# Kernel tuning notes

Measured on AMD Instinct MI355X. Metric: run time of the kernel, lower is better.

## Reference

```python
import jax, jax.numpy as jnp
import numpy as np

INV_DELTA = 15.0  # init kwarg inv_delta
EPS = 1e-12       # torch F.normalize eps


def setup_inputs() -> dict:
    key = jax.random.key(0)
    k1, k2 = jax.random.split(key)
    features = jax.random.normal(k1, (32, 256, 30, 30), dtype=jnp.float32)
    # _embedding buffer: randn clamped to >= 0
    embedding = jnp.maximum(jax.random.normal(k2, (2048, 256), dtype=jnp.float32), 0.0)
    # _min_distance_mean buffer, initialized to 0.5
    min_distance_mean = jnp.ones((1,), dtype=jnp.float32) * 0.5
    return {"features": features, "embedding": embedding,
            "min_distance_mean": min_distance_mean}


def reference(features, embedding, min_distance_mean):
    # crop 1-pixel border: [B,C,H,W] -> [B,C,H-2,W-2]
    f = features[:, :, 1:-1, 1:-1]
    # squared euclidean distance to each codeword via GEMM trick:
    # dist[b,k,h,w] = ||f[b,:,h,w]||^2 + ||e[k]||^2 - 2 <f, e[k]>
    f2 = jnp.sum(f * f, axis=1, keepdims=True)                 # [B,1,H',W']
    e2 = jnp.sum(embedding * embedding, axis=1)                # [K]
    xe = jnp.einsum('bchw,kc->bkhw', f, embedding)             # 1x1-conv GEMM
    dist = f2 + e2[None, :, None, None] - 2.0 * xe             # [B,K,H',W']
    # adaptive temperature softmax over codewords
    inv_delta_adaptive = INV_DELTA / min_distance_mean[0]
    codes = jax.nn.softmax(-inv_delta_adaptive * dist, axis=1)  # [B,K,H',W']
    # global average pool + L1 normalize
    bow = jnp.mean(codes, axis=(2, 3))                          # [B,K]
    bow = bow / jnp.maximum(jnp.sum(jnp.abs(bow), axis=1, keepdims=True), EPS)
    return (bow, codes)
```

## Files before the change

kernel.cpp:

```cpp
#include <hip/hip_runtime.h>
#include <hip/hip_bf16.h>
#include <math.h>

typedef __attribute__((ext_vector_type(8))) short bf16x8;
typedef __attribute__((ext_vector_type(16))) float f32x16;

#define B_ 32
#define C_ 256
#define K_ 2048
#define HW_ 784
#define NPIX 25088
#define FEAT_BSTRIDE 230400
#define FEAT_CSTRIDE 900
#define INV_DELTA 15.0f
#define LOG2E 1.4426950408889634f
#define QSCALE 409.6f
#define QDEC (LOG2E / QSCALE)

#define BM 128
#define BN 128
#define LSTR 40
#define NSLAB 16

__device__ __forceinline__ ushort f2bf(float x) {
    __hip_bfloat16 h = __float2bfloat16(x);
    return *reinterpret_cast<ushort*>(&h);
}
__device__ __forceinline__ float bf2f(ushort u) {
    __hip_bfloat16 h;
    *reinterpret_cast<ushort*>(&h) = u;
    return __bfloat162float(h);
}

__global__ void e2_kernel(const float* __restrict__ emb, float* __restrict__ e2) {
    int t = threadIdx.x;
    int wid = t >> 6, lane = t & 63;
    int k = blockIdx.x * 4 + wid;
    const float* er = emb + (size_t)k * C_;
    float v0 = er[lane], v1 = er[lane + 64], v2 = er[lane + 128], v3 = er[lane + 192];
    float s = v0 * v0 + v1 * v1 + v2 * v2 + v3 * v3;
#pragma unroll
    for (int off = 32; off > 0; off >>= 1) s += __shfl_xor(s, off);
    if (lane == 0) e2[k] = s;
}

__global__ void prep_e_kernel(const float* __restrict__ emb,
                              ushort* __restrict__ ehi, ushort* __restrict__ elo) {
    int i = blockIdx.x * 256 + threadIdx.x;
    float v = emb[i];
    ushort h = f2bf(v);
    float r = v - bf2f(h);
    ehi[i] = h;
    elo[i] = f2bf(r);
}

__global__ __launch_bounds__(256, 2) void gemm_kernel(
    const float* __restrict__ feat, const ushort* __restrict__ ehi,
    const ushort* __restrict__ elo, const float* __restrict__ mdm,
    const float* __restrict__ e2g, ushort* __restrict__ zq,
    float* __restrict__ m_part, float* __restrict__ l_part)
{
    __shared__ ushort Ah[BM * LSTR], Al[BM * LSTR], Bh[BN * LSTR], Bl[BN * LSTR];
    __shared__ float redA[2][132];
    __shared__ float redM[132];

    int t = threadIdx.x;
    int lane = t & 63, wid = t >> 6;
    int wrow = wid >> 1, wcol = wid & 1;
    int g = lane >> 5, ci = lane & 31;

    int px0 = blockIdx.x * BM;
    int k0  = blockIdx.y * BN;

    int apx = t & 127;
    int ahalf = t >> 7;
    int pxs = px0 + apx;
    int bs = pxs / HW_, hws = pxs % HW_;
    int hs = hws / 28, wsx = hws % 28;
    const float* fbase = feat + (size_t)bs * FEAT_BSTRIDE + (size_t)(hs + 1) * 30 + (wsx + 1);

    f32x16 acc[2][2];
#pragma unroll
    for (int mi = 0; mi < 2; ++mi)
#pragma unroll
        for (int ni = 0; ni < 2; ++ni)
            acc[mi][ni] = (f32x16)(0.0f);

    for (int kc = 0; kc < 8; ++kc) {
        int c0 = kc * 32;
        __syncthreads();
        {
            float v[16];
#pragma unroll
            for (int p = 0; p < 16; ++p)
                v[p] = fbase[(size_t)(c0 + ahalf * 16 + p) * FEAT_CSTRIDE];
#pragma unroll
            for (int o = 0; o < 2; ++o) {
                uint4 uh, ul;
                uint* uhp = reinterpret_cast<uint*>(&uh);
                uint* ulp = reinterpret_cast<uint*>(&ul);
#pragma unroll
                for (int q = 0; q < 4; ++q) {
                    float f0 = v[o * 8 + 2 * q], f1 = v[o * 8 + 2 * q + 1];
                    ushort h0 = f2bf(f0), h1 = f2bf(f1);
                    float r0 = f0 - bf2f(h0), r1 = f1 - bf2f(h1);
                    uhp[q] = (uint)h0 | ((uint)h1 << 16);
                    ulp[q] = (uint)f2bf(r0) | ((uint)f2bf(r1) << 16);
                }
                int oct = ahalf * 2 + o;
                *reinterpret_cast<uint4*>(&Ah[apx * LSTR + oct * 8]) = uh;
                *reinterpret_cast<uint4*>(&Al[apx * LSTR + oct * 8]) = ul;
            }
        }
        {
#pragma unroll
            for (int i = 0; i < 2; ++i) {
                int idx = t + i * 256;
                int kl = idx >> 2, oct = idx & 3;
                uint4 vh = *reinterpret_cast<const uint4*>(&ehi[(size_t)(k0 + kl) * C_ + c0 + oct * 8]);
                uint4 vl = *reinterpret_cast<const uint4*>(&elo[(size_t)(k0 + kl) * C_ + c0 + oct * 8]);
                *reinterpret_cast<uint4*>(&Bh[kl * LSTR + oct * 8]) = vh;
                *reinterpret_cast<uint4*>(&Bl[kl * LSTR + oct * 8]) = vl;
            }
        }
        __syncthreads();
#pragma unroll
        for (int s = 0; s < 2; ++s) {
            bf16x8 ah[2], av[2], bh[2], bv[2];
#pragma unroll
            for (int mi = 0; mi < 2; ++mi) {
                int off = (wrow * 64 + mi * 32 + ci) * LSTR + s * 16 + g * 8;
                ah[mi] = *reinterpret_cast<const bf16x8*>(&Ah[off]);
                av[mi] = *reinterpret_cast<const bf16x8*>(&Al[off]);
            }
#pragma unroll
            for (int ni = 0; ni < 2; ++ni) {
                int off = (wcol * 64 + ni * 32 + ci) * LSTR + s * 16 + g * 8;
                bh[ni] = *reinterpret_cast<const bf16x8*>(&Bh[off]);
                bv[ni] = *reinterpret_cast<const bf16x8*>(&Bl[off]);
            }
#pragma unroll
            for (int mi = 0; mi < 2; ++mi)
#pragma unroll
                for (int ni = 0; ni < 2; ++ni) {
                    acc[mi][ni] = __builtin_amdgcn_mfma_f32_32x32x16_bf16(ah[mi], bh[ni], acc[mi][ni], 0, 0, 0);
                    acc[mi][ni] = __builtin_amdgcn_mfma_f32_32x32x16_bf16(ah[mi], bv[ni], acc[mi][ni], 0, 0, 0);
                    acc[mi][ni] = __builtin_amdgcn_mfma_f32_32x32x16_bf16(av[mi], bh[ni], acc[mi][ni], 0, 0, 0);
                }
        }
    }

    const float alpha = INV_DELTA / mdm[0];
    float e2v[2];
#pragma unroll
    for (int ni = 0; ni < 2; ++ni) e2v[ni] = e2g[k0 + wcol * 64 + ni * 32 + ci];
#pragma unroll
    for (int mi = 0; mi < 2; ++mi)
#pragma unroll
        for (int ni = 0; ni < 2; ++ni)
            acc[mi][ni] = alpha * (2.0f * acc[mi][ni] - e2v[ni]);

    float ms[2][16];
    {
        float mt[2][16];
#pragma unroll
        for (int mi = 0; mi < 2; ++mi)
#pragma unroll
            for (int r = 0; r < 16; ++r)
                mt[mi][r] = fmaxf(acc[mi][0][r], acc[mi][1][r]);
#pragma unroll
        for (int off = 1; off < 32; off <<= 1)
#pragma unroll
            for (int mi = 0; mi < 2; ++mi)
#pragma unroll
                for (int r = 0; r < 16; ++r)
                    mt[mi][r] = fmaxf(mt[mi][r], __shfl_xor(mt[mi][r], off));
        if (ci == 0) {
#pragma unroll
            for (int mi = 0; mi < 2; ++mi)
#pragma unroll
                for (int r = 0; r < 16; ++r)
                    redA[wcol][wrow * 64 + mi * 32 + (r & 3) + 8 * (r >> 2) + 4 * g] = mt[mi][r];
        }
    }
    __syncthreads();
    if (t < 128) redM[t] = fmaxf(redA[0][t], redA[1][t]);
    __syncthreads();
#pragma unroll
    for (int mi = 0; mi < 2; ++mi)
#pragma unroll
        for (int r = 0; r < 16; ++r)
            ms[mi][r] = redM[wrow * 64 + mi * 32 + (r & 3) + 8 * (r >> 2) + 4 * g];

    {
        float lt[2][16];
#pragma unroll
        for (int mi = 0; mi < 2; ++mi)
#pragma unroll
            for (int r = 0; r < 16; ++r)
                lt[mi][r] = exp2f((acc[mi][0][r] - ms[mi][r]) * LOG2E) +
                            exp2f((acc[mi][1][r] - ms[mi][r]) * LOG2E);
#pragma unroll
        for (int off = 1; off < 32; off <<= 1)
#pragma unroll
            for (int mi = 0; mi < 2; ++mi)
#pragma unroll
                for (int r = 0; r < 16; ++r)
                    lt[mi][r] += __shfl_xor(lt[mi][r], off);
        if (ci == 0) {
#pragma unroll
            for (int mi = 0; mi < 2; ++mi)
#pragma unroll
                for (int r = 0; r < 16; ++r)
                    redA[wcol][wrow * 64 + mi * 32 + (r & 3) + 8 * (r >> 2) + 4 * g] = lt[mi][r];
        }
    }
    __syncthreads();
    if (t < 128) {
        int slab = blockIdx.y;
        m_part[(size_t)slab * NPIX + px0 + t] = redM[t];
        l_part[(size_t)slab * NPIX + px0 + t] = redA[0][t] + redA[1][t];
    }

#pragma unroll
    for (int mi = 0; mi < 2; ++mi)
#pragma unroll
        for (int ni = 0; ni < 2; ++ni) {
            int k = k0 + wcol * 64 + ni * 32 + ci;
#pragma unroll
            for (int r = 0; r < 16; r += 2) {
                int row = wrow * 64 + mi * 32 + (r & 3) + 8 * (r >> 2) + 4 * g;
                int pxx = px0 + row;
                int bb = pxx / HW_, hh = pxx - bb * HW_;
                float s0 = fmaxf((acc[mi][ni][r]     - ms[mi][r])     * QSCALE, -32760.f);
                float s1 = fmaxf((acc[mi][ni][r + 1] - ms[mi][r + 1]) * QSCALE, -32760.f);
                int q0 = (int)s0, q1 = (int)s1;
                uint u = ((uint)(ushort)(short)q0) | (((uint)(ushort)(short)q1) << 16);
                *reinterpret_cast<uint*>(&zq[(size_t)(bb * K_ + k) * HW_ + hh]) = u;
            }
        }
}

__global__ void combine_kernel(const float* __restrict__ m_part, const float* __restrict__ l_part,
                               float* __restrict__ m_fin, float* __restrict__ rl_g) {
    int p = blockIdx.x * 256 + threadIdx.x;
    float m = -3.4e38f;
#pragma unroll
    for (int s = 0; s < NSLAB; ++s) m = fmaxf(m, m_part[(size_t)s * NPIX + p]);
    float l = 0.f;
#pragma unroll
    for (int s = 0; s < NSLAB; ++s)
        l += l_part[(size_t)s * NPIX + p] * exp2f((m_part[(size_t)s * NPIX + p] - m) * LOG2E);
    m_fin[p] = m;
    rl_g[p] = 1.0f / l;
}

__global__ __launch_bounds__(256) void finish_kernel(
    const ushort* __restrict__ zq, const float* __restrict__ m_part,
    const float* __restrict__ m_fin, const float* __restrict__ rl_g,
    float* __restrict__ codes, float* __restrict__ bow)
{
    __shared__ float corr[HW_], rls[HW_];
    __shared__ float bsum[64][4];
    int t = threadIdx.x;
    int kc = blockIdx.x, b = blockIdx.y;
    int slab = kc >> 1;
    for (int i = t; i < HW_; i += 256) {
        int p = b * HW_ + i;
        corr[i] = (m_part[(size_t)slab * NPIX + p] - m_fin[p]) * LOG2E;
        rls[i] = rl_g[p];
    }
    __syncthreads();
    int wid = t >> 6, lane = t & 63;
    for (int kl = 0; kl < 64; ++kl) {
        int k = kc * 64 + kl;
        size_t base = ((size_t)b * K_ + k) * HW_;
        float ssum = 0.f;
        if (t < 196) {
            uint2 raw = *reinterpret_cast<const uint2*>(&zq[base + t * 4]);
            int q0 = (int)(short)(raw.x & 0xffffu), q1 = (int)(short)(raw.x >> 16);
            int q2 = (int)(short)(raw.y & 0xffffu), q3 = (int)(short)(raw.y >> 16);
            float4 out;
            out.x = exp2f(fmaf((float)q0, QDEC, corr[t * 4 + 0])) * rls[t * 4 + 0];
            out.y = exp2f(fmaf((float)q1, QDEC, corr[t * 4 + 1])) * rls[t * 4 + 1];
            out.z = exp2f(fmaf((float)q2, QDEC, corr[t * 4 + 2])) * rls[t * 4 + 2];
            out.w = exp2f(fmaf((float)q3, QDEC, corr[t * 4 + 3])) * rls[t * 4 + 3];
            *reinterpret_cast<float4*>(&codes[base + t * 4]) = out;
            ssum = out.x + out.y + out.z + out.w;
        }
#pragma unroll
        for (int off = 32; off > 0; off >>= 1) ssum += __shfl_xor(ssum, off);
        if (lane == 0) bsum[kl][wid] = ssum;
    }
    __syncthreads();
    if (t < 64) {
        float s = bsum[t][0] + bsum[t][1] + bsum[t][2] + bsum[t][3];
        bow[(size_t)b * K_ + kc * 64 + t] = s * (1.0f / 784.0f);
    }
}

__global__ void bownorm_kernel(float* __restrict__ bow) {
    __shared__ float wred[4];
    __shared__ float denom_s;
    int b = blockIdx.x, t = threadIdx.x;
    float* row = bow + (size_t)b * K_;
    float v[8];
    float s = 0.f;
#pragma unroll
    for (int i = 0; i < 8; ++i) {
        v[i] = row[t + i * 256];
        s += fabsf(v[i]);
    }
#pragma unroll
    for (int off = 32; off > 0; off >>= 1) s += __shfl_xor(s, off);
    int wid = t >> 6, lane = t & 63;
    if (lane == 0) wred[wid] = s;
    __syncthreads();
    if (t == 0) denom_s = fmaxf(wred[0] + wred[1] + wred[2] + wred[3], 1e-12f);
    __syncthreads();
    float denom = denom_s;
#pragma unroll
    for (int i = 0; i < 8; ++i) row[t + i * 256] = v[i] / denom;
}

extern "C" void kernel_launch(void* const* d_in, const int* in_sizes, int n_in,
                              void* d_out, int out_size, void* d_ws, size_t ws_size,
                              hipStream_t stream) {
    const float* feat = (const float*)d_in[0];
    const float* emb  = (const float*)d_in[1];
    const float* mdm  = (const float*)d_in[2];
    float* bow   = (float*)d_out;
    float* codes = bow + (size_t)B_ * K_;

    char* ws = (char*)d_ws;
    size_t off = 0;
    auto alloc = [&](size_t bytes) { char* p = ws + off; off = (off + bytes + 255) & ~(size_t)255; return p; };
    ushort* ehi   = (ushort*)alloc((size_t)K_ * C_ * 2);
    ushort* elo   = (ushort*)alloc((size_t)K_ * C_ * 2);
    float*  e2    = (float*)alloc(K_ * 4);
    float*  m_part = (float*)alloc((size_t)NSLAB * NPIX * 4);
    float*  l_part = (float*)alloc((size_t)NSLAB * NPIX * 4);
    float*  m_fin = (float*)alloc((size_t)NPIX * 4);
    float*  rl_g  = (float*)alloc((size_t)NPIX * 4);
    ushort* zq    = (ushort*)alloc((size_t)NPIX * K_ * 2);

    e2_kernel<<<512, 256, 0, stream>>>(emb, e2);
    prep_e_kernel<<<2048, 256, 0, stream>>>(emb, ehi, elo);
    gemm_kernel<<<dim3(196, 16), 256, 0, stream>>>(feat, ehi, elo, mdm, e2, zq, m_part, l_part);
    combine_kernel<<<98, 256, 0, stream>>>(m_part, l_part, m_fin, rl_g);
    finish_kernel<<<dim3(32, 32), 256, 0, stream>>>(zq, m_part, m_fin, rl_g, codes, bow);
    bownorm_kernel<<<32, 256, 0, stream>>>(bow);
}
```

Measured before the change: 259.5 us.

## Pre-split features to bf16 hi/lo and stream GEMM tiles via direct global-to-LDS loads

Adds a prep kernel that transposes the cropped features into pixel-major bf16 hi/lo arrays, stored temporarily in the codes output buffer. The GEMM then loads all A and B tiles with global_load_lds into XOR-swizzled LDS rows of 64 elements, using a K-step of 64 channels. This replaces the strided fp32 gathers and the split conversion that were repeated in each of the 16 k-slab blocks. The block index is also remapped so that slabs sharing a pixel tile are scheduled together for L2 reuse. The cost is an extra kernel pass and larger LDS tiles, which may lower occupancy.

```diff
diff --git a/kernel.cpp b/kernel.cpp
--- a/kernel.cpp
+++ b/kernel.cpp
@@ -19,8 +19,11 @@
 
 #define BM 128
 #define BN 128
-#define LSTR 40
+#define LSTR 64
 #define NSLAB 16
+
+#define AS1 __attribute__((address_space(1)))
+#define AS3 __attribute__((address_space(3)))
 
 __device__ __forceinline__ ushort f2bf(float x) {
     __hip_bfloat16 h = __float2bfloat16(x);
@@ -30,6 +33,9 @@
     __hip_bfloat16 h;
     *reinterpret_cast<ushort*>(&h) = u;
     return __bfloat162float(h);
+}
+__device__ __forceinline__ void gl_lds16(const ushort* g, ushort* l) {
+    __builtin_amdgcn_global_load_lds((AS1 const uint*)g, (AS3 uint*)l, 16, 0, 0);
 }
 
 __global__ void e2_kernel(const float* __restrict__ emb, float* __restrict__ e2) {
@@ -54,13 +60,53 @@
     elo[i] = f2bf(r);
 }
 
+__global__ __launch_bounds__(256) void prep_f_kernel(const float* __restrict__ feat,
+                                                     ushort* __restrict__ fhi,
+                                                     ushort* __restrict__ flo) {
+    __shared__ float F[256 * 65];
+    int t = threadIdx.x;
+    int px0 = blockIdx.x * 64;
+    {
+        int lane = t & 63, cq = t >> 6;
+        int px = px0 + lane;
+        int b = px / HW_, hw = px % HW_;
+        int h = hw / 28, w = hw % 28;
+        const float* base = feat + (size_t)b * FEAT_BSTRIDE + (size_t)(h + 1) * 30 + (w + 1);
+#pragma unroll
+        for (int cc = 0; cc < 64; ++cc) {
+            int c = cq * 64 + cc;
+            F[c * 65 + lane] = base[(size_t)c * FEAT_CSTRIDE];
+        }
+    }
+    __syncthreads();
+    {
+        int px_l = t >> 2, cseg = t & 3;
+        size_t ob = (size_t)(px0 + px_l) * C_ + cseg * 64;
+        uint uh[32], ul[32];
+#pragma unroll
+        for (int j = 0; j < 32; ++j) {
+            float v0 = F[(cseg * 64 + 2 * j) * 65 + px_l];
+            float v1 = F[(cseg * 64 + 2 * j + 1) * 65 + px_l];
+            ushort h0 = f2bf(v0), h1 = f2bf(v1);
+            float r0 = v0 - bf2f(h0), r1 = v1 - bf2f(h1);
+            uh[j] = (uint)h0 | ((uint)h1 << 16);
+            ul[j] = (uint)f2bf(r0) | ((uint)f2bf(r1) << 16);
+        }
+#pragma unroll
+        for (int j = 0; j < 8; ++j) {
+            *reinterpret_cast<uint4*>(&fhi[ob + j * 8]) = *reinterpret_cast<uint4*>(&uh[j * 4]);
+            *reinterpret_cast<uint4*>(&flo[ob + j * 8]) = *reinterpret_cast<uint4*>(&ul[j * 4]);
+        }
+    }
+}
+
 __global__ __launch_bounds__(256, 2) void gemm_kernel(
-    const float* __restrict__ feat, const ushort* __restrict__ ehi,
-    const ushort* __restrict__ elo, const float* __restrict__ mdm,
-    const float* __restrict__ e2g, ushort* __restrict__ zq,
-    float* __restrict__ m_part, float* __restrict__ l_part)
+    const ushort* __restrict__ fhi, const ushort* __restrict__ flo,
+    const ushort* __restrict__ ehi, const ushort* __restrict__ elo,
+    const float* __restrict__ mdm, const float* __restrict__ e2g,
+    ushort* __restrict__ zq, float* __restrict__ m_part, float* __restrict__ l_part)
 {
-    __shared__ ushort Ah[BM * LSTR], Al[BM * LSTR], Bh[BN * LSTR], Bl[BN * LSTR];
+    __shared__ __align__(16) ushort Ah[BM * LSTR], Al[BM * LSTR], Bh[BN * LSTR], Bl[BN * LSTR];
     __shared__ float redA[2][132];
     __shared__ float redM[132];
 
@@ -69,15 +115,11 @@
     int wrow = wid >> 1, wcol = wid & 1;
     int g = lane >> 5, ci = lane & 31;
 
-    int px0 = blockIdx.x * BM;
-    int k0  = blockIdx.y * BN;
-
-    int apx = t & 127;
-    int ahalf = t >> 7;
-    int pxs = px0 + apx;
-    int bs = pxs / HW_, hws = pxs % HW_;
-    int hs = hws / 28, wsx = hws % 28;
-    const float* fbase = feat + (size_t)bs * FEAT_BSTRIDE + (size_t)(hs + 1) * 30 + (wsx + 1);
+    int bid = blockIdx.x;
+    int swz = (bid & 7) * 392 + (bid >> 3);
+    int tile = swz >> 4, slab = swz & 15;
+    int px0 = tile * BM;
+    int k0 = slab * BN;
 
     f32x16 acc[2][2];
 #pragma unroll
@@ -86,56 +128,37 @@
         for (int ni = 0; ni < 2; ++ni)
             acc[mi][ni] = (f32x16)(0.0f);
 
-    for (int kc = 0; kc < 8; ++kc) {
-        int c0 = kc * 32;
+    for (int step = 0; step < 4; ++step) {
+        int c0 = step * 64;
         __syncthreads();
-        {
-            float v[16];
-#pragma unroll
-            for (int p = 0; p < 16; ++p)
-                v[p] = fbase[(size_t)(c0 + ahalf * 16 + p) * FEAT_CSTRIDE];
-#pragma unroll
-            for (int o = 0; o < 2; ++o) {
-                uint4 uh, ul;
-                uint* uhp = reinterpret_cast<uint*>(&uh);
-                uint* ulp = reinterpret_cast<uint*>(&ul);
-#pragma unroll
-                for (int q = 0; q < 4; ++q) {
-                    float f0 = v[o * 8 + 2 * q], f1 = v[o * 8 + 2 * q + 1];
-                    ushort h0 = f2bf(f0), h1 = f2bf(f1);
-                    float r0 = f0 - bf2f(h0), r1 = f1 - bf2f(h1);
-                    uhp[q] = (uint)h0 | ((uint)h1 << 16);
-                    ulp[q] = (uint)f2bf(r0) | ((uint)f2bf(r1) << 16);
-                }
-                int oct = ahalf * 2 + o;
-                *reinterpret_cast<uint4*>(&Ah[apx * LSTR + oct * 8]) = uh;
-                *reinterpret_cast<uint4*>(&Al[apx * LSTR + oct * 8]) = ul;
-            }
-        }
-        {
-#pragma unroll
-            for (int i = 0; i < 2; ++i) {
-                int idx = t + i * 256;
-                int kl = idx >> 2, oct = idx & 3;
-                uint4 vh = *reinterpret_cast<const uint4*>(&ehi[(size_t)(k0 + kl) * C_ + c0 + oct * 8]);
-                uint4 vl = *reinterpret_cast<const uint4*>(&elo[(size_t)(k0 + kl) * C_ + c0 + oct * 8]);
-                *reinterpret_cast<uint4*>(&Bh[kl * LSTR + oct * 8]) = vh;
-                *reinterpret_cast<uint4*>(&Bl[kl * LSTR + oct * 8]) = vl;
-            }
+#pragma unroll
+        for (int i = 0; i < 4; ++i) {
+            int unit = t + i * 256;
+            int row = unit >> 3;
+            int usw = (unit & 7) ^ (row & 7);
+            size_t ga = (size_t)(px0 + row) * C_ + c0 + usw * 8;
+            size_t gb = (size_t)(k0 + row) * C_ + c0 + usw * 8;
+            gl_lds16(fhi + ga, &Ah[unit * 8]);
+            gl_lds16(flo + ga, &Al[unit * 8]);
+            gl_lds16(ehi + gb, &Bh[unit * 8]);
+            gl_lds16(elo + gb, &Bl[unit * 8]);
         }
         __syncthreads();
-#pragma unroll
-        for (int s = 0; s < 2; ++s) {
+
+        int x7 = ci & 7;
+#pragma unroll
+        for (int s = 0; s < 4; ++s) {
+            int ucol = ((2 * s + g) ^ x7) * 8;
             bf16x8 ah[2], av[2], bh[2], bv[2];
 #pragma unroll
             for (int mi = 0; mi < 2; ++mi) {
-                int off = (wrow * 64 + mi * 32 + ci) * LSTR + s * 16 + g * 8;
+                int off = (wrow * 64 + mi * 32 + ci) * LSTR + ucol;
                 ah[mi] = *reinterpret_cast<const bf16x8*>(&Ah[off]);
                 av[mi] = *reinterpret_cast<const bf16x8*>(&Al[off]);
             }
 #pragma unroll
             for (int ni = 0; ni < 2; ++ni) {
-                int off = (wcol * 64 + ni * 32 + ci) * LSTR + s * 16 + g * 8;
+                int off = (wcol * 64 + ni * 32 + ci) * LSTR + ucol;
                 bh[ni] = *reinterpret_cast<const bf16x8*>(&Bh[off]);
                 bv[ni] = *reinterpret_cast<const bf16x8*>(&Bl[off]);
             }
@@ -217,7 +240,6 @@
     }
     __syncthreads();
     if (t < 128) {
-        int slab = blockIdx.y;
         m_part[(size_t)slab * NPIX + px0 + t] = redM[t];
         l_part[(size_t)slab * NPIX + px0 + t] = redA[0][t] + redA[1][t];
     }
@@ -335,18 +357,22 @@
     char* ws = (char*)d_ws;
     size_t off = 0;
     auto alloc = [&](size_t bytes) { char* p = ws + off; off = (off + bytes + 255) & ~(size_t)255; return p; };
-    ushort* ehi   = (ushort*)alloc((size_t)K_ * C_ * 2);
-    ushort* elo   = (ushort*)alloc((size_t)K_ * C_ * 2);
-    float*  e2    = (float*)alloc(K_ * 4);
+    ushort* ehi    = (ushort*)alloc((size_t)K_ * C_ * 2);
+    ushort* elo    = (ushort*)alloc((size_t)K_ * C_ * 2);
+    float*  e2     = (float*)alloc(K_ * 4);
     float*  m_part = (float*)alloc((size_t)NSLAB * NPIX * 4);
     float*  l_part = (float*)alloc((size_t)NSLAB * NPIX * 4);
-    float*  m_fin = (float*)alloc((size_t)NPIX * 4);
-    float*  rl_g  = (float*)alloc((size_t)NPIX * 4);
-    ushort* zq    = (ushort*)alloc((size_t)NPIX * K_ * 2);
+    float*  m_fin  = (float*)alloc((size_t)NPIX * 4);
+    float*  rl_g   = (float*)alloc((size_t)NPIX * 4);
+    ushort* zq     = (ushort*)alloc((size_t)NPIX * K_ * 2);
+
+    ushort* fhi = (ushort*)codes;
+    ushort* flo = fhi + (size_t)NPIX * C_;
 
     e2_kernel<<<512, 256, 0, stream>>>(emb, e2);
     prep_e_kernel<<<2048, 256, 0, stream>>>(emb, ehi, elo);
-    gemm_kernel<<<dim3(196, 16), 256, 0, stream>>>(feat, ehi, elo, mdm, e2, zq, m_part, l_part);
+    prep_f_kernel<<<392, 256, 0, stream>>>(feat, fhi, flo);
+    gemm_kernel<<<3136, 256, 0, stream>>>(fhi, flo, ehi, elo, mdm, e2, zq, m_part, l_part);
     combine_kernel<<<98, 256, 0, stream>>>(m_part, l_part, m_fin, rl_g);
     finish_kernel<<<dim3(32, 32), 256, 0, stream>>>(zq, m_part, m_fin, rl_g, codes, bow);
     bownorm_kernel<<<32, 256, 0, stream>>>(bow);
```

Measured after the change: 275.7 us. 1.06x slower.
